# Kernel tuning notes

Hardware: AMD Instinct MI355X
Metric: run time of the kernel (lower is better)

## Reference

```python
import jax, jax.numpy as jnp
import numpy as np

DIM, HEADS, DHEAD = 256, 8, 64
HID = HEADS * DHEAD


def _elu1(x):
    # F.elu(x) + 1 == exp(x) for x<0, x+1 for x>=0
    return jnp.where(x > 0, x + 1.0, jnp.exp(x))


def setup_inputs() -> dict:
    key = jax.random.key(0)
    ks = jax.random.split(key, 6)
    B, H, W = 8, 64, 64
    x = jax.random.normal(ks[0], (B, DIM, H, W), dtype=jnp.float32)
    contact_map = jax.random.uniform(ks[1], (B, 1, H, W), dtype=jnp.float32)
    s_qkv = 1.0 / np.sqrt(DIM)
    Wqkv = jax.random.normal(ks[2], (3 * HID, DIM), dtype=jnp.float32) * s_qkv
    s_out = 1.0 / np.sqrt(HID)
    Wout = jax.random.normal(ks[3], (DIM, HID), dtype=jnp.float32) * s_out
    bout = jax.random.normal(ks[4], (DIM,), dtype=jnp.float32) * 0.01
    contact_scale = jnp.float32(0.1)
    return {"x": x, "contact_map": contact_map, "Wqkv": Wqkv,
            "Wout": Wout, "bout": bout, "contact_scale": contact_scale}


def reference(x, contact_map, Wqkv, Wout, bout, contact_scale):
    b, c, h, w = x.shape
    n = h * w
    xf = x.reshape(b, c, n)                                  # b c n
    qkv = jnp.einsum('oc,bcn->bon', Wqkv, xf)                # b (3*H*D) n
    qkv = qkv.reshape(b, 3, HEADS, DHEAD, n)                 # qkv-major channel order
    q = _elu1(qkv[:, 0])                                     # b h d n
    k = _elu1(qkv[:, 1])
    v = qkv[:, 2]
    cm = contact_map.reshape(b, 1, 1, n)                     # b 1 1 n
    k = k * (1.0 + contact_scale * cm)
    kv = jnp.einsum('bhdn,bhen->bhde', k, v)                 # b h d e
    ksum = k.sum(axis=-1)                                    # b h d
    z = 1.0 / (jnp.einsum('bhdn,bhd->bhn', q, ksum) + 1e-6)  # b h n
    out = jnp.einsum('bhde,bhdn->bhne', kv, q) * z[..., None]  # b h n e
    out = out.transpose(0, 1, 3, 2).reshape(b, HID, n)       # b (h d) n
    y = jnp.einsum('oc,bcn->bon', Wout, out) + bout[None, :, None]
    return y.reshape(b, -1, h, w)
```

## Files before the change

### kernel.cpp

```cpp
#include <hip/hip_runtime.h>
#include <stdint.h>


#define NPIX 4096
#define HIDC 512
#define DIMC 256
#define BATCH 8

typedef __attribute__((ext_vector_type(8))) short bf16x8;
typedef __attribute__((ext_vector_type(4))) float f32x4;
typedef __attribute__((ext_vector_type(16))) float f32x16;

__device__ __forceinline__ float bf2f(unsigned short h) {
    unsigned int u = ((unsigned int)h) << 16; float f;
    __builtin_memcpy(&f, &u, 4); return f;
}
__device__ __forceinline__ unsigned short f2bf(float f) {
    unsigned int u; __builtin_memcpy(&u, &f, 4);
    u += 0x7fffu + ((u >> 16) & 1u);
    return (unsigned short)(u >> 16);
}
__device__ __forceinline__ float elu1(float x) {
    return x > 0.f ? x + 1.f : __expf(x);
}
__device__ __forceinline__ void gl16(const unsigned short* g, unsigned short* l) {
    __builtin_amdgcn_global_load_lds(
        (__attribute__((address_space(1))) const void*)g,
        (__attribute__((address_space(3))) void*)l, 16, 0, 0);
}

__global__ __launch_bounds__(256) void k_convW(
    const float* __restrict__ Wqkv, const float* __restrict__ Wout,
    unsigned short* __restrict__ Wb, unsigned short* __restrict__ Wob)
{
    int i4 = (blockIdx.x * 256 + threadIdx.x) * 4;
    const int NW1 = 1536 * 256;
    float4 v; unsigned short* dst;
    if (i4 < NW1) { v = *(const float4*)&Wqkv[i4]; dst = Wb + i4; }
    else { int j = i4 - NW1; v = *(const float4*)&Wout[j]; dst = Wob + j; }
    ushort4 o; o.x = f2bf(v.x); o.y = f2bf(v.y); o.z = f2bf(v.z); o.w = f2bf(v.w);
    *(ushort4*)dst = o;
}

__global__ __launch_bounds__(256) void k_tx(
    const float* __restrict__ x, unsigned short* __restrict__ xT)
{
    __shared__ float tile[32][33];
    const int n0 = blockIdx.x * 32, c0 = blockIdx.y * 32, b = blockIdx.z;
    const int t = threadIdx.x;
    const int r = t >> 3, c4 = (t & 7) * 4;
    float4 v = *(const float4*)&x[((size_t)b * DIMC + c0 + r) * NPIX + n0 + c4];
    tile[r][c4 + 0] = v.x; tile[r][c4 + 1] = v.y;
    tile[r][c4 + 2] = v.z; tile[r][c4 + 3] = v.w;
    __syncthreads();
    ushort4 o;
    unsigned short* op = (unsigned short*)&o;
#pragma unroll
    for (int i = 0; i < 4; i++) op[i] = f2bf(tile[c4 + i][r]);
    *(ushort4*)&xT[((size_t)b * NPIX + n0 + r) * DIMC + c0 + c4] = o;
}

__global__ __launch_bounds__(256) void k_qkv(
    const unsigned short* __restrict__ xT,
    const unsigned short* __restrict__ Wb,
    const float* __restrict__ cmp,
    const float* __restrict__ csp,
    unsigned short* __restrict__ qT,
    unsigned short* __restrict__ kb,
    unsigned short* __restrict__ vb)
{
    const int b  = blockIdx.z;
    const int m0 = blockIdx.x * 128;
    const int n0 = blockIdx.y * 128;
    const int t = threadIdx.x;
    const int wave = t >> 6, lane = t & 63;
    const int wm = wave >> 1, wn = wave & 1;
    const int l31 = lane & 31, lhi = lane >> 5;
    const int sect = n0 >> 9;

    __shared__ unsigned short As[128 * 64];
    __shared__ unsigned short Bs[128 * 64];

    const unsigned short* Ag = xT + ((size_t)b * NPIX + m0) * DIMC;
    const unsigned short* Bg = Wb + (size_t)n0 * DIMC;

    const unsigned short* mArr = (sect == 0) ? As : Bs;
    const unsigned short* nArr = (sect == 0) ? Bs : As;

    f32x16 acc[2][2];
#pragma unroll
    for (int i = 0; i < 2; i++)
#pragma unroll
        for (int j = 0; j < 2; j++)
#pragma unroll
            for (int r = 0; r < 16; r++) acc[i][j][r] = 0.f;

    const int r8  = lane >> 3;
    const int jg8 = (((lane & 7) ^ r8) & 7) * 8;
    const int xsw = (l31 & 7);

    for (int k0 = 0; k0 < DIMC; k0 += 64) {
#pragma unroll
        for (int i = 0; i < 4; i++) {
            const int rowg = wave * 32 + i * 8;
            gl16(&Ag[(size_t)(rowg + r8) * DIMC + k0 + jg8], &As[rowg * 64]);
            gl16(&Bg[(size_t)(rowg + r8) * DIMC + k0 + jg8], &Bs[rowg * 64]);
        }
        __syncthreads();
#pragma unroll
        for (int ks = 0; ks < 4; ks++) {
            const int coff = ((ks * 2 + lhi) ^ xsw) * 8;
            bf16x8 af[2], bfg[2];
#pragma unroll
            for (int fm = 0; fm < 2; fm++)
                af[fm] = *(const bf16x8*)&mArr[(wm * 64 + fm * 32 + l31) * 64 + coff];
#pragma unroll
            for (int fn = 0; fn < 2; fn++)
                bfg[fn] = *(const bf16x8*)&nArr[(wn * 64 + fn * 32 + l31) * 64 + coff];
#pragma unroll
            for (int fm = 0; fm < 2; fm++)
#pragma unroll
                for (int fn = 0; fn < 2; fn++)
                    acc[fm][fn] = __builtin_amdgcn_mfma_f32_32x32x16_bf16(
                        af[fm], bfg[fn], acc[fm][fn], 0, 0, 0);
        }
        __syncthreads();
    }

    const float cs = *csp;
    if (sect == 0) {
#pragma unroll
        for (int fm = 0; fm < 2; fm++) {
            const int pbase = m0 + wm * 64 + fm * 32;
#pragma unroll
            for (int fn = 0; fn < 2; fn++) {
                const int o = n0 + wn * 64 + fn * 32 + l31;
#pragma unroll
                for (int r = 0; r < 16; r++) {
                    int prow = pbase + (r & 3) + 8 * (r >> 2) + 4 * lhi;
                    qT[((size_t)b * NPIX + prow) * HIDC + o] = f2bf(elu1(acc[fm][fn][r]));
                }
            }
        }
    } else {
        unsigned short* dstb = (sect == 1) ? kb : vb;
#pragma unroll
        for (int fm = 0; fm < 2; fm++) {
            const int obase = (n0 & 511) + wm * 64 + fm * 32;
#pragma unroll
            for (int fn = 0; fn < 2; fn++) {
                const int pixel = m0 + wn * 64 + fn * 32 + l31;
                float g = 1.f;
                if (sect == 1) g = 1.f + cs * cmp[(size_t)b * NPIX + pixel];
#pragma unroll
                for (int r = 0; r < 16; r++) {
                    int orow = obase + (r & 3) + 8 * (r >> 2) + 4 * lhi;
                    float val = acc[fm][fn][r];
                    if (sect == 1) val = elu1(val) * g;
                    dstb[((size_t)b * HIDC + orow) * NPIX + pixel] = f2bf(val);
                }
            }
        }
    }
}

#define LKV 72
__global__ __launch_bounds__(256) void k_kv(
    const unsigned short* __restrict__ kb, const unsigned short* __restrict__ vb,
    float* __restrict__ kvT,
    float* __restrict__ ksum)
{
    const int bh = blockIdx.y, nc = blockIdx.x;
    const int t = threadIdx.x, wave = t >> 6, lane = t & 63;
    const int lrow = lane & 15, quad = lane >> 4;

    __shared__ unsigned short ks[64 * LKV];
    __shared__ unsigned short vs[64 * LKV];

    const size_t base = (size_t)bh * 64 * NPIX;
    f32x4 acc[4];
#pragma unroll
    for (int i = 0; i < 4; i++) acc[i] = (f32x4){0.f, 0.f, 0.f, 0.f};
    float ksacc = 0.f;

    const int row = t >> 2, c8 = (t & 3) * 8;

    for (int step = 0; step < 8; step++) {
        const int ncol = nc * 512 + step * 64;
        const size_t g = base + (size_t)row * NPIX + ncol;
        uint4 k0 = *(const uint4*)&kb[g + c8];
        uint4 k1 = *(const uint4*)&kb[g + c8 + 32];
        *(uint4*)&ks[row * LKV + c8]      = k0;
        *(uint4*)&ks[row * LKV + c8 + 32] = k1;
        *(uint4*)&vs[row * LKV + c8]      = *(const uint4*)&vb[g + c8];
        *(uint4*)&vs[row * LKV + c8 + 32] = *(const uint4*)&vb[g + c8 + 32];
        const unsigned short* kp0 = (const unsigned short*)&k0;
        const unsigned short* kp1 = (const unsigned short*)&k1;
#pragma unroll
        for (int j = 0; j < 8; j++) ksacc += bf2f(kp0[j]) + bf2f(kp1[j]);
        __syncthreads();
#pragma unroll
        for (int ks32 = 0; ks32 < 2; ks32++) {
            bf16x8 bfv = *(const bf16x8*)&vs[(wave * 16 + lrow) * LKV + ks32 * 32 + quad * 8];
#pragma unroll
            for (int mt = 0; mt < 4; mt++) {
                bf16x8 af = *(const bf16x8*)&ks[(mt * 16 + lrow) * LKV + ks32 * 32 + quad * 8];
                acc[mt] = __builtin_amdgcn_mfma_f32_16x16x32_bf16(af, bfv, acc[mt], 0, 0, 0);
            }
        }
        __syncthreads();
    }

    float* kvb = kvT + (size_t)bh * 4096;
#pragma unroll
    for (int mt = 0; mt < 4; mt++)
#pragma unroll
        for (int r = 0; r < 4; r++)
            atomicAdd(&kvb[(wave * 16 + lrow) * 64 + mt * 16 + quad * 4 + r], acc[mt][r]);
    atomicAdd(&ksum[bh * 64 + row], ksacc);
}

__global__ __launch_bounds__(256) void k_oy(
    const unsigned short* __restrict__ qT,
    const float* __restrict__ kvT,
    const float* __restrict__ ksum,
    const unsigned short* __restrict__ Wob,
    const float* __restrict__ bout,
    float* __restrict__ y)
{
    const int p0 = blockIdx.x * 128, oh = blockIdx.y, b = blockIdx.z;
    const int t = threadIdx.x, wave = t >> 6, lane = t & 63;
    const int l31 = lane & 31, lhi = lane >> 5;
    const int wm = wave >> 1, wn = wave & 1;

    __shared__ unsigned short Aq[128 * 72];
    __shared__ unsigned short Bv[96 * 72];
    __shared__ unsigned short Wo[128 * 64];

    for (int i = t; i < 30 * 64; i += 256)
        Bv[(66 + (i >> 6)) * 72 + (i & 63)] = 0;

    f32x16 acc2[2][2];
#pragma unroll
    for (int i = 0; i < 2; i++)
#pragma unroll
        for (int j = 0; j < 2; j++)
#pragma unroll
            for (int r = 0; r < 16; r++) acc2[i][j][r] = 0.f;

    for (int h = 0; h < 8; h++) {
        const int bh = b * 8 + h;
        const unsigned short* qg = qT + ((size_t)b * NPIX + p0) * HIDC + h * 64;
#pragma unroll
        for (int i = 0; i < 4; i++) {
            int idx = t + i * 256;
            int row = idx >> 3, c8 = (idx & 7) * 8;
            *(uint4*)&Aq[row * 72 + c8] = *(const uint4*)&qg[(size_t)row * HIDC + c8];
        }
        const float* kvg = kvT + (size_t)bh * 4096;
#pragma unroll
        for (int i = 0; i < 4; i++) {
            int idx = t + i * 256;
            int e = idx >> 4, d4 = (idx & 15) * 4;
            float4 v = *(const float4*)&kvg[e * 64 + d4];
            ushort4 o; o.x = f2bf(v.x); o.y = f2bf(v.y); o.z = f2bf(v.z); o.w = f2bf(v.w);
            *(ushort4*)&Bv[e * 72 + d4] = o;
        }
        if (t < 64) {
            float ksv = ksum[bh * 64 + t];
            unsigned short hi = f2bf(ksv);
            Bv[64 * 72 + t] = hi;
            Bv[65 * 72 + t] = f2bf(ksv - bf2f(hi));
        }
#pragma unroll
        for (int i = 0; i < 4; i++) {
            int idx = t + i * 256;
            int o = idx >> 3, c = idx & 7;
            *(uint4*)&Wo[o * 64 + ((c ^ (o & 7)) * 8)] =
                *(const uint4*)&Wob[(size_t)(oh * 128 + o) * HIDC + h * 64 + c * 8];
        }
        __syncthreads();

        f32x16 a1[3];
#pragma unroll
        for (int j = 0; j < 3; j++)
#pragma unroll
            for (int r = 0; r < 16; r++) a1[j][r] = 0.f;
#pragma unroll
        for (int ksb = 0; ksb < 4; ksb++) {
            int koff = ksb * 16 + lhi * 8;
            bf16x8 af = *(const bf16x8*)&Aq[(wave * 32 + l31) * 72 + koff];
#pragma unroll
            for (int nf = 0; nf < 3; nf++) {
                bf16x8 bg = *(const bf16x8*)&Bv[(nf * 32 + l31) * 72 + koff];
                a1[nf] = __builtin_amdgcn_mfma_f32_32x32x16_bf16(af, bg, a1[nf], 0, 0, 0);
            }
        }
        __syncthreads();

#pragma unroll
        for (int r = 0; r < 16; r++) {
            float hi = __shfl(a1[2][r], lane & 32);
            float lo = __shfl(a1[2][r], (lane & 32) | 1);
            float z = 1.f / (hi + lo + 1e-6f);
            int prow = (r & 3) + 8 * (r >> 2) + 4 * lhi;
#pragma unroll
            for (int nf = 0; nf < 2; nf++)
                Aq[(wave * 32 + prow) * 72 + nf * 32 + l31] = f2bf(a1[nf][r] * z);
        }
        __syncthreads();

#pragma unroll
        for (int ksb = 0; ksb < 4; ksb++) {
            int koff = ksb * 16 + lhi * 8;
            bf16x8 bg[2];
#pragma unroll
            for (int fn = 0; fn < 2; fn++)
                bg[fn] = *(const bf16x8*)&Aq[(wn * 64 + fn * 32 + l31) * 72 + koff];
            int wchunk = ((ksb * 2 + lhi) ^ (l31 & 7)) * 8;
#pragma unroll
            for (int fm = 0; fm < 2; fm++) {
                bf16x8 ag = *(const bf16x8*)&Wo[(wm * 64 + fm * 32 + l31) * 64 + wchunk];
#pragma unroll
                for (int fn = 0; fn < 2; fn++)
                    acc2[fm][fn] = __builtin_amdgcn_mfma_f32_32x32x16_bf16(
                        ag, bg[fn], acc2[fm][fn], 0, 0, 0);
            }
        }
        __syncthreads();
    }

#pragma unroll
    for (int fm = 0; fm < 2; fm++) {
#pragma unroll
        for (int r = 0; r < 16; r++) {
            int orow = oh * 128 + wm * 64 + fm * 32 + (r & 3) + 8 * (r >> 2) + 4 * lhi;
            float bias = bout[orow];
#pragma unroll
            for (int fn = 0; fn < 2; fn++)
                y[((size_t)b * DIMC + orow) * NPIX + p0 + wn * 64 + fn * 32 + l31] =
                    acc2[fm][fn][r] + bias;
        }
    }
}

extern "C" void kernel_launch(void* const* d_in, const int* in_sizes, int n_in,
                              void* d_out, int out_size, void* d_ws, size_t ws_size,
                              hipStream_t stream) {
    (void)in_sizes; (void)n_in; (void)out_size; (void)ws_size;
    const float* x    = (const float*)d_in[0];
    const float* cm   = (const float*)d_in[1];
    const float* Wqkv = (const float*)d_in[2];
    const float* Wout = (const float*)d_in[3];
    const float* bout = (const float*)d_in[4];
    const float* csp  = (const float*)d_in[5];
    float* y = (float*)d_out;

    const size_t qn = (size_t)BATCH * HIDC * NPIX;
    char* ws = (char*)d_ws;
    unsigned short* qT  = (unsigned short*)ws;                  ws += qn * 2;
    unsigned short* kb  = (unsigned short*)ws;                  ws += qn * 2;
    unsigned short* vb  = (unsigned short*)ws;                  ws += qn * 2;
    unsigned short* xT  = (unsigned short*)ws;                  ws += qn * 2;
    float* kvp   = (float*)ws;                                  ws += (size_t)64 * 64 * 64 * 4;
    float* ksump = (float*)ws;                                  ws += (size_t)64 * 64 * 4;
    unsigned short* Wb  = (unsigned short*)ws;                  ws += (size_t)1536 * 256 * 2;
    unsigned short* Wob = (unsigned short*)ws;

    hipMemsetAsync(kvp, 0, ((size_t)64 * 64 * 64 + 64 * 64) * sizeof(float), stream);
    k_convW<<<512, 256, 0, stream>>>(Wqkv, Wout, Wb, Wob);
    k_tx  <<<dim3(128, 8, 8), 256, 0, stream>>>(x, xT);
    k_qkv <<<dim3(32, 12, 8), 256, 0, stream>>>(xT, Wb, cm, csp, qT, kb, vb);
    k_kv  <<<dim3(8, 64),     256, 0, stream>>>(kb, vb, kvp, ksump);
    k_oy  <<<dim3(32, 2, 8),  256, 0, stream>>>(qT, kvp, ksump, Wob, bout, y);
}
```

Measured before the change: 234.0 us.

## Prefetch next head's tiles into registers and split kv reduction across more blocks

k_oy now loads the next head's q, kv, ksum and Wout tiles into registers while computing the current head, with a separate Ao buffer so staged writes overlap the MMAs. The denominator MFMA uses a zero-filled fragment instead of zeroing padded LDS rows. k_kv is register double-buffered, launched with twice as many column chunks, and writes kv transposed so k_oy transposes during conversion. This hides global load latency and raises occupancy for the kv kernel, at the cost of extra registers, more LDS, more atomics, and scattered 2-byte LDS stores for the kv transpose.

```diff
diff --git a/kernel.cpp b/kernel.cpp
--- a/kernel.cpp
+++ b/kernel.cpp
@@ -167,7 +167,7 @@
 #define LKV 72
 __global__ __launch_bounds__(256) void k_kv(
     const unsigned short* __restrict__ kb, const unsigned short* __restrict__ vb,
-    float* __restrict__ kvT,
+    float* __restrict__ kv,
     float* __restrict__ ksum)
 {
     const int bh = blockIdx.y, nc = blockIdx.x;
@@ -184,20 +184,31 @@
     float ksacc = 0.f;
 
     const int row = t >> 2, c8 = (t & 3) * 8;
-
-    for (int step = 0; step < 8; step++) {
-        const int ncol = nc * 512 + step * 64;
-        const size_t g = base + (size_t)row * NPIX + ncol;
-        uint4 k0 = *(const uint4*)&kb[g + c8];
-        uint4 k1 = *(const uint4*)&kb[g + c8 + 32];
-        *(uint4*)&ks[row * LKV + c8]      = k0;
-        *(uint4*)&ks[row * LKV + c8 + 32] = k1;
-        *(uint4*)&vs[row * LKV + c8]      = *(const uint4*)&vb[g + c8];
-        *(uint4*)&vs[row * LKV + c8 + 32] = *(const uint4*)&vb[g + c8 + 32];
-        const unsigned short* kp0 = (const unsigned short*)&k0;
-        const unsigned short* kp1 = (const unsigned short*)&k1;
-#pragma unroll
-        for (int j = 0; j < 8; j++) ksacc += bf2f(kp0[j]) + bf2f(kp1[j]);
+    const size_t g0 = base + (size_t)row * NPIX + nc * 256;
+
+    uint4 ka0 = *(const uint4*)&kb[g0 + c8];
+    uint4 ka1 = *(const uint4*)&kb[g0 + c8 + 32];
+    uint4 va0 = *(const uint4*)&vb[g0 + c8];
+    uint4 va1 = *(const uint4*)&vb[g0 + c8 + 32];
+
+    for (int step = 0; step < 4; step++) {
+        *(uint4*)&ks[row * LKV + c8]      = ka0;
+        *(uint4*)&ks[row * LKV + c8 + 32] = ka1;
+        *(uint4*)&vs[row * LKV + c8]      = va0;
+        *(uint4*)&vs[row * LKV + c8 + 32] = va1;
+        {
+            const unsigned short* kp0 = (const unsigned short*)&ka0;
+            const unsigned short* kp1 = (const unsigned short*)&ka1;
+#pragma unroll
+            for (int j = 0; j < 8; j++) ksacc += bf2f(kp0[j]) + bf2f(kp1[j]);
+        }
+        if (step < 3) {
+            const size_t g = g0 + (step + 1) * 64;
+            ka0 = *(const uint4*)&kb[g + c8];
+            ka1 = *(const uint4*)&kb[g + c8 + 32];
+            va0 = *(const uint4*)&vb[g + c8];
+            va1 = *(const uint4*)&vb[g + c8 + 32];
+        }
         __syncthreads();
 #pragma unroll
         for (int ks32 = 0; ks32 < 2; ks32++) {
@@ -211,18 +222,18 @@
         __syncthreads();
     }
 
-    float* kvb = kvT + (size_t)bh * 4096;
+    float* kvb = kv + (size_t)bh * 4096;
 #pragma unroll
     for (int mt = 0; mt < 4; mt++)
 #pragma unroll
         for (int r = 0; r < 4; r++)
-            atomicAdd(&kvb[(wave * 16 + lrow) * 64 + mt * 16 + quad * 4 + r], acc[mt][r]);
+            atomicAdd(&kvb[(mt * 16 + quad * 4 + r) * 64 + wave * 16 + lrow], acc[mt][r]);
     atomicAdd(&ksum[bh * 64 + row], ksacc);
 }
 
 __global__ __launch_bounds__(256) void k_oy(
     const unsigned short* __restrict__ qT,
-    const float* __restrict__ kvT,
+    const float* __restrict__ kv,
     const float* __restrict__ ksum,
     const unsigned short* __restrict__ Wob,
     const float* __restrict__ bout,
@@ -234,12 +245,10 @@
     const int wm = wave >> 1, wn = wave & 1;
 
     __shared__ unsigned short Aq[128 * 72];
-    __shared__ unsigned short Bv[96 * 72];
+    __shared__ unsigned short Ao[128 * 72];
+    __shared__ unsigned short Bv[66 * 72];
     __shared__ unsigned short Wo[128 * 64];
 
-    for (int i = t; i < 30 * 64; i += 256)
-        Bv[(66 + (i >> 6)) * 72 + (i & 63)] = 0;
-
     f32x16 acc2[2][2];
 #pragma unroll
     for (int i = 0; i < 2; i++)
@@ -248,67 +257,99 @@
 #pragma unroll
             for (int r = 0; r < 16; r++) acc2[i][j][r] = 0.f;
 
+    uint4 qr[4]; float4 kvr[4]; uint4 wr[4]; float ksr = 0.f;
+
+#define LOAD_REGS(h)                                                            \
+    {                                                                           \
+        const unsigned short* qg = qT + ((size_t)b * NPIX + p0) * HIDC + (h) * 64; \
+        _Pragma("unroll")                                                       \
+        for (int i = 0; i < 4; i++) {                                           \
+            int idx = t + i * 256;                                              \
+            qr[i] = *(const uint4*)&qg[(size_t)(idx >> 3) * HIDC + (idx & 7) * 8]; \
+        }                                                                       \
+        const float* kvg = kv + (size_t)(b * 8 + (h)) * 4096;                   \
+        _Pragma("unroll")                                                       \
+        for (int i = 0; i < 4; i++) {                                           \
+            int idx = t + i * 256;                                              \
+            kvr[i] = *(const float4*)&kvg[(idx >> 4) * 64 + (idx & 15) * 4];    \
+        }                                                                       \
+        const unsigned short* wg = Wob + (size_t)(oh * 128) * HIDC + (h) * 64;  \
+        _Pragma("unroll")                                                       \
+        for (int i = 0; i < 4; i++) {                                           \
+            int idx = t + i * 256;                                              \
+            wr[i] = *(const uint4*)&wg[(size_t)(idx >> 3) * HIDC + (idx & 7) * 8]; \
+        }                                                                       \
+        if (t < 64) ksr = ksum[(b * 8 + (h)) * 64 + t];                         \
+    }
+
+#define WRITE_AB()                                                              \
+    {                                                                           \
+        _Pragma("unroll")                                                       \
+        for (int i = 0; i < 4; i++) {                                           \
+            int idx = t + i * 256;                                              \
+            *(uint4*)&Aq[(idx >> 3) * 72 + (idx & 7) * 8] = qr[i];              \
+        }                                                                       \
+        _Pragma("unroll")                                                       \
+        for (int i = 0; i < 4; i++) {                                           \
+            int idx = t + i * 256;                                              \
+            int d = idx >> 4, e4 = (idx & 15) * 4;                              \
+            const float* f4 = (const float*)&kvr[i];                            \
+            _Pragma("unroll")                                                   \
+            for (int j = 0; j < 4; j++) Bv[(e4 + j) * 72 + d] = f2bf(f4[j]);    \
+        }                                                                       \
+        if (t < 64) {                                                           \
+            unsigned short hi = f2bf(ksr);                                      \
+            Bv[64 * 72 + t] = hi;                                               \
+            Bv[65 * 72 + t] = f2bf(ksr - bf2f(hi));                             \
+        }                                                                       \
+    }
+
+#define WRITE_W()                                                               \
+    {                                                                           \
+        _Pragma("unroll")                                                       \
+        for (int i = 0; i < 4; i++) {                                           \
+            int idx = t + i * 256;                                              \
+            int o = idx >> 3, c = idx & 7;                                      \
+            *(uint4*)&Wo[o * 64 + ((c ^ (o & 7)) * 8)] = wr[i];                 \
+        }                                                                       \
+    }
+
+    LOAD_REGS(0);
+    WRITE_AB();
+    WRITE_W();
+
     for (int h = 0; h < 8; h++) {
-        const int bh = b * 8 + h;
-        const unsigned short* qg = qT + ((size_t)b * NPIX + p0) * HIDC + h * 64;
-#pragma unroll
-        for (int i = 0; i < 4; i++) {
-            int idx = t + i * 256;
-            int row = idx >> 3, c8 = (idx & 7) * 8;
-            *(uint4*)&Aq[row * 72 + c8] = *(const uint4*)&qg[(size_t)row * HIDC + c8];
-        }
-        const float* kvg = kvT + (size_t)bh * 4096;
-#pragma unroll
-        for (int i = 0; i < 4; i++) {
-            int idx = t + i * 256;
-            int e = idx >> 4, d4 = (idx & 15) * 4;
-            float4 v = *(const float4*)&kvg[e * 64 + d4];
-            ushort4 o; o.x = f2bf(v.x); o.y = f2bf(v.y); o.z = f2bf(v.z); o.w = f2bf(v.w);
-            *(ushort4*)&Bv[e * 72 + d4] = o;
-        }
-        if (t < 64) {
-            float ksv = ksum[bh * 64 + t];
-            unsigned short hi = f2bf(ksv);
-            Bv[64 * 72 + t] = hi;
-            Bv[65 * 72 + t] = f2bf(ksv - bf2f(hi));
-        }
-#pragma unroll
-        for (int i = 0; i < 4; i++) {
-            int idx = t + i * 256;
-            int o = idx >> 3, c = idx & 7;
-            *(uint4*)&Wo[o * 64 + ((c ^ (o & 7)) * 8)] =
-                *(const uint4*)&Wob[(size_t)(oh * 128 + o) * HIDC + h * 64 + c * 8];
-        }
-        __syncthreads();
-
-        f32x16 a1[3];
-#pragma unroll
-        for (int j = 0; j < 3; j++)
-#pragma unroll
-            for (int r = 0; r < 16; r++) a1[j][r] = 0.f;
+        __syncthreads();
+        if (h < 7) LOAD_REGS(h + 1);
+
+        f32x16 a1[2], aden;
+#pragma unroll
+        for (int r = 0; r < 16; r++) { a1[0][r] = 0.f; a1[1][r] = 0.f; aden[r] = 0.f; }
 #pragma unroll
         for (int ksb = 0; ksb < 4; ksb++) {
             int koff = ksb * 16 + lhi * 8;
             bf16x8 af = *(const bf16x8*)&Aq[(wave * 32 + l31) * 72 + koff];
 #pragma unroll
-            for (int nf = 0; nf < 3; nf++) {
+            for (int nf = 0; nf < 2; nf++) {
                 bf16x8 bg = *(const bf16x8*)&Bv[(nf * 32 + l31) * 72 + koff];
                 a1[nf] = __builtin_amdgcn_mfma_f32_32x32x16_bf16(af, bg, a1[nf], 0, 0, 0);
             }
-        }
-        __syncthreads();
-
+            bf16x8 bd = (bf16x8)(short)0;
+            if (l31 < 2) bd = *(const bf16x8*)&Bv[(64 + l31) * 72 + koff];
+            aden = __builtin_amdgcn_mfma_f32_32x32x16_bf16(af, bd, aden, 0, 0, 0);
+        }
 #pragma unroll
         for (int r = 0; r < 16; r++) {
-            float hi = __shfl(a1[2][r], lane & 32);
-            float lo = __shfl(a1[2][r], (lane & 32) | 1);
+            float hi = __shfl(aden[r], lane & 32);
+            float lo = __shfl(aden[r], (lane & 32) | 1);
             float z = 1.f / (hi + lo + 1e-6f);
             int prow = (r & 3) + 8 * (r >> 2) + 4 * lhi;
 #pragma unroll
             for (int nf = 0; nf < 2; nf++)
-                Aq[(wave * 32 + prow) * 72 + nf * 32 + l31] = f2bf(a1[nf][r] * z);
-        }
-        __syncthreads();
+                Ao[(wave * 32 + prow) * 72 + nf * 32 + l31] = f2bf(a1[nf][r] * z);
+        }
+        __syncthreads();
+        if (h < 7) WRITE_AB();
 
 #pragma unroll
         for (int ksb = 0; ksb < 4; ksb++) {
@@ -316,7 +357,7 @@
             bf16x8 bg[2];
 #pragma unroll
             for (int fn = 0; fn < 2; fn++)
-                bg[fn] = *(const bf16x8*)&Aq[(wn * 64 + fn * 32 + l31) * 72 + koff];
+                bg[fn] = *(const bf16x8*)&Ao[(wn * 64 + fn * 32 + l31) * 72 + koff];
             int wchunk = ((ksb * 2 + lhi) ^ (l31 & 7)) * 8;
 #pragma unroll
             for (int fm = 0; fm < 2; fm++) {
@@ -328,6 +369,7 @@
             }
         }
         __syncthreads();
+        if (h < 7) WRITE_W();
     }
 
 #pragma unroll
@@ -342,6 +384,9 @@
                     acc2[fm][fn][r] + bias;
         }
     }
+#undef LOAD_REGS
+#undef WRITE_AB
+#undef WRITE_W
 }
 
 extern "C" void kernel_launch(void* const* d_in, const int* in_sizes, int n_in,
@@ -371,6 +416,6 @@
     k_convW<<<512, 256, 0, stream>>>(Wqkv, Wout, Wb, Wob);
     k_tx  <<<dim3(128, 8, 8), 256, 0, stream>>>(x, xT);
     k_qkv <<<dim3(32, 12, 8), 256, 0, stream>>>(xT, Wb, cm, csp, qT, kb, vb);
-    k_kv  <<<dim3(8, 64),     256, 0, stream>>>(kb, vb, kvp, ksump);
+    k_kv  <<<dim3(16, 64),    256, 0, stream>>>(kb, vb, kvp, ksump);
     k_oy  <<<dim3(32, 2, 8),  256, 0, stream>>>(qT, kvp, ksump, Wob, bout, y);
 }
```

New measurement: 279.5 us. 1.19x slower.
